# Performance work log

Measured on AMD Instinct MI355X. Metric: run time of the kernel, lower is better.

The kernel has to match this reference:

```python
import jax, jax.numpy as jnp
import numpy as np

BS = 4096
D = 256
TAU = 0.5
EPS = 1e-08          # eps added to negative-sum denominator (module arg)
COS_EPS = 1e-08      # nn.CosineSimilarity norm clamp


def setup_inputs() -> dict:
    key = jax.random.key(0)
    k1, k2 = jax.random.split(key)
    zi = jax.random.normal(k1, (BS, D), dtype=jnp.float32)
    zj = jax.random.normal(k2, (BS, D), dtype=jnp.float32)
    return {"zi": zi, "zj": zj}


def reference(zi, zj):
    bs = zi.shape[0]
    n = 2 * bs
    z = jnp.concatenate([zi, zj], axis=0)                       # [2bs, D]
    # cosine similarity = normalized dot products (norms clamped like torch)
    norm = jnp.linalg.norm(z, axis=-1, keepdims=True)
    zn = z / jnp.maximum(norm, COS_EPS)
    sim = jnp.matmul(zn, zn.T) / TAU                            # [2bs, 2bs]
    e = jnp.exp(sim)
    # positive pairs: row i pairs with column (i+bs) mod 2bs
    rows = jnp.arange(n)
    pair = jnp.concatenate([jnp.arange(bs) + bs, jnp.arange(bs)])
    sim_pos = e[rows, pair]                                     # [2bs]
    # negatives: all entries in a row except the diagonal
    sim_neg_sum = e.sum(axis=-1) - jnp.diagonal(e)              # [2bs]
    loss = jnp.mean(-jnp.log(sim_pos / (sim_neg_sum + EPS)))
    return loss
```

## Files before the change

kernel.cpp:

```cpp
#include <hip/hip_runtime.h>
#include <hip/hip_bf16.h>


#define N_ROWS 8192
#define BSZ    4096
#define DIM    256
#define INV_TAU 2.0f
#define EPS_REF 1e-8f
#define COS_EPS 1e-8f
#define NG2     64
#define NBLK2   (NG2 * (NG2 + 1) / 2)

typedef __attribute__((ext_vector_type(4))) float f32x4;
typedef long long i64;
typedef union { int4 v; i64 d[2]; } pack16;

__global__ __launch_bounds__(256) void knorm(const float* __restrict__ zi,
                                             const float* __restrict__ zj,
                                             unsigned char* __restrict__ znsw,
                                             float* __restrict__ out) {
    __shared__ float lds[4096];
    __shared__ float nrm[16];
    const int rg = blockIdx.x;
    const int t  = threadIdx.x;
    const int row0 = rg * 16;
    if (rg == 0 && t == 0) out[0] = 0.f;

    #pragma unroll
    for (int s = 0; s < 4; ++s) {
        const int e = s * 1024 + t * 4;
        const int r = row0 + (e >> 8);
        const int k = e & 255;
        const float* src = (r < BSZ) ? zi + (size_t)r * DIM + k
                                     : zj + (size_t)(r - BSZ) * DIM + k;
        *(float4*)&lds[e] = *(const float4*)src;
    }
    __syncthreads();

    {
        const int r = t >> 4, p = t & 15;
        float ss = 0.f;
        #pragma unroll
        for (int j = 0; j < 16; ++j) { const float x = lds[r * 256 + p * 16 + j]; ss += x * x; }
        ss += __shfl_xor(ss, 1); ss += __shfl_xor(ss, 2);
        ss += __shfl_xor(ss, 4); ss += __shfl_xor(ss, 8);
        if (p == 0) nrm[r] = 1.0f / fmaxf(sqrtf(ss), COS_EPS);
    }
    __syncthreads();

    const int kbp = t >> 6, fl = t & 63;
    const int r16 = fl & 15, q = fl >> 4;
    const float inv = nrm[r16];
    int w[4];
    #pragma unroll
    for (int h = 0; h < 2; ++h) {
        const int kk = (2 * kbp + h) * 32 + q * 8;
        float f[8];
        #pragma unroll
        for (int j = 0; j < 8; ++j) f[j] = lds[r16 * 256 + kk + j] * inv;
        int a = 0, b = 0;
        a = __builtin_amdgcn_cvt_pk_fp8_f32(f[0], f[1], a, false);
        a = __builtin_amdgcn_cvt_pk_fp8_f32(f[2], f[3], a, true);
        b = __builtin_amdgcn_cvt_pk_fp8_f32(f[4], f[5], b, false);
        b = __builtin_amdgcn_cvt_pk_fp8_f32(f[6], f[7], b, true);
        w[h * 2] = a; w[h * 2 + 1] = b;
    }
    *(int4*)(znsw + ((size_t)(rg * 4 + kbp) * 64 + fl) * 16) = make_int4(w[0], w[1], w[2], w[3]);
}

__global__ __launch_bounds__(256, 2) void kgemm(const unsigned char* __restrict__ znsw,
                                                float* __restrict__ P,
                                                float* __restrict__ selfdot,
                                                float* __restrict__ pairdot) {
    __shared__ __align__(16) unsigned char pan[2][32768];
    const int w = threadIdx.x >> 6;
    const int l = threadIdx.x & 63;

    const int t = blockIdx.x;
    int Gi = (int)((129.0f - sqrtf(16641.0f - 8.0f * (float)t)) * 0.5f);
    while ((Gi + 1) * (129 - (Gi + 1)) / 2 <= t) ++Gi;
    while (Gi * (129 - Gi) / 2 > t) --Gi;
    const int Gj = Gi + (t - Gi * (129 - Gi) / 2);

    const char* srcA = (const char*)znsw + (size_t)Gi * 32768;
    const char* srcB = (const char*)znsw + (size_t)Gj * 32768;
    #pragma unroll
    for (int sub = 0; sub < 8; ++sub) {
        const int off = sub * 4096 + w * 1024;
        __builtin_amdgcn_global_load_lds(
            (const __attribute__((address_space(1))) void*)(srcA + off + l * 16),
            (__attribute__((address_space(3))) void*)(&pan[0][off]), 16, 0, 0);
        __builtin_amdgcn_global_load_lds(
            (const __attribute__((address_space(1))) void*)(srcB + off + l * 16),
            (__attribute__((address_space(3))) void*)(&pan[1][off]), 16, 0, 0);
    }
    __syncthreads();

    const int rh = w >> 1, ch = w & 1;
    const char* Ap = (const char*)&pan[0][0] + rh * 16384 + l * 16;
    const char* Bp = (const char*)&pan[1][0] + ch * 16384 + l * 16;

    f32x4 acc[4][4];
    #pragma unroll
    for (int mt = 0; mt < 4; ++mt)
        #pragma unroll
        for (int nt = 0; nt < 4; ++nt)
            acc[mt][nt] = (f32x4){0.f, 0.f, 0.f, 0.f};

    #pragma unroll
    for (int kbp = 0; kbp < 4; ++kbp) {
        pack16 a4[4], b4[4];
        #pragma unroll
        for (int mt = 0; mt < 4; ++mt) a4[mt].v = *(const int4*)(Ap + (mt * 4 + kbp) * 1024);
        #pragma unroll
        for (int nt = 0; nt < 4; ++nt) b4[nt].v = *(const int4*)(Bp + (nt * 4 + kbp) * 1024);
        #pragma unroll
        for (int mt = 0; mt < 4; ++mt)
            #pragma unroll
            for (int nt = 0; nt < 4; ++nt) {
                acc[mt][nt] = __builtin_amdgcn_mfma_f32_16x16x32_fp8_fp8(
                    a4[mt].d[0], b4[nt].d[0], acc[mt][nt], 0, 0, 0);
                acc[mt][nt] = __builtin_amdgcn_mfma_f32_16x16x32_fp8_fp8(
                    a4[mt].d[1], b4[nt].d[1], acc[mt][nt], 0, 0, 0);
            }
    }

    const int c = l & 15, q = l >> 4;
    const int rsel = c - 4 * q;
    const bool vld = (rsel >= 0) && (rsel < 4);

    if ((Gi == Gj || Gj == Gi + 32) && rh == ch) {
        float dv[4];
        #pragma unroll
        for (int mt = 0; mt < 4; ++mt) {
            float d = acc[mt][mt][0];
            #pragma unroll
            for (int r = 1; r < 4; ++r)
                if (rsel == r) d = acc[mt][mt][r];
            dv[mt] = d;
        }
        if (vld) {
            float* dst = (Gi == Gj) ? selfdot : pairdot;
            #pragma unroll
            for (int mt = 0; mt < 4; ++mt)
                dst[Gi * 128 + rh * 64 + mt * 16 + c] = dv[mt];
        }
    }

    #pragma unroll
    for (int mt = 0; mt < 4; ++mt)
        #pragma unroll
        for (int nt = 0; nt < 4; ++nt)
            #pragma unroll
            for (int r = 0; r < 4; ++r)
                acc[mt][nt][r] = __expf(acc[mt][nt][r] * INV_TAU);

    float rs[4][4];
    #pragma unroll
    for (int mt = 0; mt < 4; ++mt)
        #pragma unroll
        for (int r = 0; r < 4; ++r)
            rs[mt][r] = acc[mt][0][r] + acc[mt][1][r] + acc[mt][2][r] + acc[mt][3][r];
    #pragma unroll
    for (int off = 1; off <= 8; off <<= 1)
        #pragma unroll
        for (int mt = 0; mt < 4; ++mt)
            #pragma unroll
            for (int r = 0; r < 4; ++r)
                rs[mt][r] += __shfl_xor(rs[mt][r], off);
    if (c == 0) {
        #pragma unroll
        for (int mt = 0; mt < 4; ++mt) {
            const f32x4 o4 = (f32x4){rs[mt][0], rs[mt][1], rs[mt][2], rs[mt][3]};
            __builtin_nontemporal_store(o4,
                (f32x4*)&P[(size_t)(Gj * 2 + ch) * N_ROWS + Gi * 128 + rh * 64 + mt * 16 + q * 4]);
        }
    }

    if (Gi != Gj) {
        float cs[4];
        #pragma unroll
        for (int nt = 0; nt < 4; ++nt) {
            float s = 0.f;
            #pragma unroll
            for (int mt = 0; mt < 4; ++mt)
                #pragma unroll
                for (int r = 0; r < 4; ++r)
                    s += acc[mt][nt][r];
            s += __shfl_xor(s, 16);
            s += __shfl_xor(s, 32);
            cs[nt] = s;
        }
        if (q == 0) {
            #pragma unroll
            for (int nt = 0; nt < 4; ++nt)
                __builtin_nontemporal_store(cs[nt],
                    &P[(size_t)(Gi * 2 + rh) * N_ROWS + Gj * 128 + ch * 64 + nt * 16 + c]);
        }
    }
}

__global__ __launch_bounds__(256) void kfinal(const float* __restrict__ P,
                                              const float* __restrict__ selfdot,
                                              const float* __restrict__ pairdot,
                                              float* __restrict__ out) {
    const int l = threadIdx.x & 63;
    const int w = threadIdx.x >> 6;
    const int row = blockIdx.x * 64 + l;
    float s = 0.f;
    #pragma unroll
    for (int st = 0; st < 32; ++st)
        s += P[(size_t)(w * 32 + st) * N_ROWS + row];
    __shared__ float wsum[4][64];
    wsum[w][l] = s;
    __syncthreads();
    if (w == 0) {
        const float tot = wsum[0][l] + wsum[1][l] + wsum[2][l] + wsum[3][l];
        const float selfe = __expf(selfdot[row] * INV_TAU);
        const float pd    = pairdot[(row < BSZ) ? row : row - BSZ];
        float loss = logf(tot - selfe + EPS_REF) - pd * INV_TAU;
        #pragma unroll
        for (int off = 32; off >= 1; off >>= 1) loss += __shfl_xor(loss, off);
        if (l == 0) atomicAdd(out, loss * (1.0f / (float)N_ROWS));
    }
}

extern "C" void kernel_launch(void* const* d_in, const int* in_sizes, int n_in,
                              void* d_out, int out_size, void* d_ws, size_t ws_size,
                              hipStream_t stream) {
    const float* zi = (const float*)d_in[0];
    const float* zj = (const float*)d_in[1];
    float* out = (float*)d_out;

    char* ws = (char*)d_ws;
    unsigned char* znsw = (unsigned char*)ws;
    float* P       = (float*)(ws + 2 * 1024 * 1024);
    float* selfdot = (float*)(ws + 6 * 1024 * 1024);
    float* pairdot = (float*)(ws + 6 * 1024 * 1024 + 32 * 1024);

    knorm <<<N_ROWS / 16, 256, 0, stream>>>(zi, zj, znsw, out);
    kgemm <<<NBLK2, 256, 0, stream>>>(znsw, P, selfdot, pairdot);
    kfinal<<<N_ROWS / 64, 256, 0, stream>>>(P, selfdot, pairdot, out);
}
```

Before: 89.43 us.

## Fuse norm, GEMM and final reduction into one cooperative persistent kernel

Replaces the three separate launches (normalize/quantize, FP8 GEMM+exp row sums, final loss reduction) with a single cooperative kernel of 512 persistent blocks, separated by grid-wide syncs. The GEMM tiles are looped over with a triangular index computation. The intent is to remove the per-kernel launch overhead and tail gaps. The cost is two grid barriers, fewer blocks than tiles (so up to five tile iterations per block with a barrier between them), and plain instead of nontemporal stores. The original three-kernel path is kept as a fallback if the cooperative launch fails.

```diff
diff --git a/kernel.cpp b/kernel.cpp
--- a/kernel.cpp
+++ b/kernel.cpp
@@ -1,5 +1,8 @@
 #include <hip/hip_runtime.h>
 #include <hip/hip_bf16.h>
+#include <hip/hip_cooperative_groups.h>
+
+namespace cg = cooperative_groups;
 
 
 #define N_ROWS 8192
@@ -9,11 +12,226 @@
 #define EPS_REF 1e-8f
 #define COS_EPS 1e-8f
 #define NG2     64
-#define NBLK2   (NG2 * (NG2 + 1) / 2)
+#define NTILES  (NG2 * (NG2 + 1) / 2)
+#define GRID    512
 
 typedef __attribute__((ext_vector_type(4))) float f32x4;
 typedef long long i64;
 typedef union { int4 v; i64 d[2]; } pack16;
+
+__global__ __launch_bounds__(256, 2) void kfused(const float* __restrict__ zi,
+                                                 const float* __restrict__ zj,
+                                                 unsigned char* __restrict__ znsw,
+                                                 float* __restrict__ P,
+                                                 float* __restrict__ selfdot,
+                                                 float* __restrict__ pairdot,
+                                                 float* __restrict__ out) {
+    __shared__ union {
+        struct { float lds[4096]; float nrm[16]; } p1;
+        struct { unsigned char pan[2][32768]; } p3;
+        struct { float wsum[4][64]; } p5;
+    } sm;
+
+    const int bid = blockIdx.x;
+    const int tid = threadIdx.x;
+    const int w   = tid >> 6;
+    const int l   = tid & 63;
+    cg::grid_group grid = cg::this_grid();
+
+    {
+        const int rg = bid;
+        const int row0 = rg * 16;
+        if (rg == 0 && tid == 0) out[0] = 0.f;
+
+        #pragma unroll
+        for (int s = 0; s < 4; ++s) {
+            const int e = s * 1024 + tid * 4;
+            const int r = row0 + (e >> 8);
+            const int k = e & 255;
+            const float* src = (r < BSZ) ? zi + (size_t)r * DIM + k
+                                         : zj + (size_t)(r - BSZ) * DIM + k;
+            *(float4*)&sm.p1.lds[e] = *(const float4*)src;
+        }
+        __syncthreads();
+        {
+            const int r = tid >> 4, p = tid & 15;
+            float ss = 0.f;
+            #pragma unroll
+            for (int j = 0; j < 16; ++j) { const float x = sm.p1.lds[r * 256 + p * 16 + j]; ss += x * x; }
+            ss += __shfl_xor(ss, 1); ss += __shfl_xor(ss, 2);
+            ss += __shfl_xor(ss, 4); ss += __shfl_xor(ss, 8);
+            if (p == 0) sm.p1.nrm[r] = 1.0f / fmaxf(sqrtf(ss), COS_EPS);
+        }
+        __syncthreads();
+        const int kbp = tid >> 6, fl = tid & 63;
+        const int r16 = fl & 15, q = fl >> 4;
+        const float inv = sm.p1.nrm[r16];
+        int wd[4];
+        #pragma unroll
+        for (int h = 0; h < 2; ++h) {
+            const int kk = (2 * kbp + h) * 32 + q * 8;
+            float f[8];
+            #pragma unroll
+            for (int j = 0; j < 8; ++j) f[j] = sm.p1.lds[r16 * 256 + kk + j] * inv;
+            int a = 0, b = 0;
+            a = __builtin_amdgcn_cvt_pk_fp8_f32(f[0], f[1], a, false);
+            a = __builtin_amdgcn_cvt_pk_fp8_f32(f[2], f[3], a, true);
+            b = __builtin_amdgcn_cvt_pk_fp8_f32(f[4], f[5], b, false);
+            b = __builtin_amdgcn_cvt_pk_fp8_f32(f[6], f[7], b, true);
+            wd[h * 2] = a; wd[h * 2 + 1] = b;
+        }
+        __syncthreads();
+        *(int4*)(znsw + ((size_t)(rg * 4 + kbp) * 64 + fl) * 16) =
+            make_int4(wd[0], wd[1], wd[2], wd[3]);
+    }
+
+    grid.sync();
+
+    for (int t = bid; t < NTILES; t += GRID) {
+        int Gi = (int)((129.0f - sqrtf(16641.0f - 8.0f * (float)t)) * 0.5f);
+        while ((Gi + 1) * (129 - (Gi + 1)) / 2 <= t) ++Gi;
+        while (Gi * (129 - Gi) / 2 > t) --Gi;
+        const int Gj = Gi + (t - Gi * (129 - Gi) / 2);
+
+        const char* srcA = (const char*)znsw + (size_t)Gi * 32768;
+        const char* srcB = (const char*)znsw + (size_t)Gj * 32768;
+        #pragma unroll
+        for (int sub = 0; sub < 8; ++sub) {
+            const int off = sub * 4096 + w * 1024;
+            __builtin_amdgcn_global_load_lds(
+                (const __attribute__((address_space(1))) void*)(srcA + off + l * 16),
+                (__attribute__((address_space(3))) void*)(&sm.p3.pan[0][off]), 16, 0, 0);
+            __builtin_amdgcn_global_load_lds(
+                (const __attribute__((address_space(1))) void*)(srcB + off + l * 16),
+                (__attribute__((address_space(3))) void*)(&sm.p3.pan[1][off]), 16, 0, 0);
+        }
+        __syncthreads();
+
+        const int rh = w >> 1, ch = w & 1;
+        const char* Ap = (const char*)&sm.p3.pan[0][0] + rh * 16384 + l * 16;
+        const char* Bp = (const char*)&sm.p3.pan[1][0] + ch * 16384 + l * 16;
+
+        f32x4 acc[4][4];
+        #pragma unroll
+        for (int mt = 0; mt < 4; ++mt)
+            #pragma unroll
+            for (int nt = 0; nt < 4; ++nt)
+                acc[mt][nt] = (f32x4){0.f, 0.f, 0.f, 0.f};
+
+        #pragma unroll
+        for (int kbp = 0; kbp < 4; ++kbp) {
+            pack16 a4[4], b4[4];
+            #pragma unroll
+            for (int mt = 0; mt < 4; ++mt) a4[mt].v = *(const int4*)(Ap + (mt * 4 + kbp) * 1024);
+            #pragma unroll
+            for (int nt = 0; nt < 4; ++nt) b4[nt].v = *(const int4*)(Bp + (nt * 4 + kbp) * 1024);
+            #pragma unroll
+            for (int mt = 0; mt < 4; ++mt)
+                #pragma unroll
+                for (int nt = 0; nt < 4; ++nt) {
+                    acc[mt][nt] = __builtin_amdgcn_mfma_f32_16x16x32_fp8_fp8(
+                        a4[mt].d[0], b4[nt].d[0], acc[mt][nt], 0, 0, 0);
+                    acc[mt][nt] = __builtin_amdgcn_mfma_f32_16x16x32_fp8_fp8(
+                        a4[mt].d[1], b4[nt].d[1], acc[mt][nt], 0, 0, 0);
+                }
+        }
+
+        const int c = l & 15, q = l >> 4;
+        const int rsel = c - 4 * q;
+        const bool vld = (rsel >= 0) && (rsel < 4);
+
+        if ((Gi == Gj || Gj == Gi + 32) && rh == ch) {
+            float dv[4];
+            #pragma unroll
+            for (int mt = 0; mt < 4; ++mt) {
+                float d = acc[mt][mt][0];
+                #pragma unroll
+                for (int r = 1; r < 4; ++r)
+                    if (rsel == r) d = acc[mt][mt][r];
+                dv[mt] = d;
+            }
+            if (vld) {
+                float* dst = (Gi == Gj) ? selfdot : pairdot;
+                #pragma unroll
+                for (int mt = 0; mt < 4; ++mt)
+                    dst[Gi * 128 + rh * 64 + mt * 16 + c] = dv[mt];
+            }
+        }
+
+        #pragma unroll
+        for (int mt = 0; mt < 4; ++mt)
+            #pragma unroll
+            for (int nt = 0; nt < 4; ++nt)
+                #pragma unroll
+                for (int r = 0; r < 4; ++r)
+                    acc[mt][nt][r] = __expf(acc[mt][nt][r] * INV_TAU);
+
+        float rs[4][4];
+        #pragma unroll
+        for (int mt = 0; mt < 4; ++mt)
+            #pragma unroll
+            for (int r = 0; r < 4; ++r)
+                rs[mt][r] = acc[mt][0][r] + acc[mt][1][r] + acc[mt][2][r] + acc[mt][3][r];
+        #pragma unroll
+        for (int off = 1; off <= 8; off <<= 1)
+            #pragma unroll
+            for (int mt = 0; mt < 4; ++mt)
+                #pragma unroll
+                for (int r = 0; r < 4; ++r)
+                    rs[mt][r] += __shfl_xor(rs[mt][r], off);
+        if (c == 0) {
+            #pragma unroll
+            for (int mt = 0; mt < 4; ++mt) {
+                const f32x4 o4 = (f32x4){rs[mt][0], rs[mt][1], rs[mt][2], rs[mt][3]};
+                *(f32x4*)&P[(size_t)(Gj * 2 + ch) * N_ROWS + Gi * 128 + rh * 64 + mt * 16 + q * 4] = o4;
+            }
+        }
+
+        if (Gi != Gj) {
+            float cs[4];
+            #pragma unroll
+            for (int nt = 0; nt < 4; ++nt) {
+                float s = 0.f;
+                #pragma unroll
+                for (int mt = 0; mt < 4; ++mt)
+                    #pragma unroll
+                    for (int r = 0; r < 4; ++r)
+                        s += acc[mt][nt][r];
+                s += __shfl_xor(s, 16);
+                s += __shfl_xor(s, 32);
+                cs[nt] = s;
+            }
+            if (q == 0) {
+                #pragma unroll
+                for (int nt = 0; nt < 4; ++nt)
+                    P[(size_t)(Gi * 2 + rh) * N_ROWS + Gj * 128 + ch * 64 + nt * 16 + c] = cs[nt];
+            }
+        }
+        __syncthreads();
+    }
+
+    grid.sync();
+
+    if (bid < N_ROWS / 64) {
+        const int row = bid * 64 + l;
+        float s = 0.f;
+        #pragma unroll
+        for (int st = 0; st < 32; ++st)
+            s += P[(size_t)(w * 32 + st) * N_ROWS + row];
+        sm.p5.wsum[w][l] = s;
+        __syncthreads();
+        if (w == 0) {
+            const float tot = sm.p5.wsum[0][l] + sm.p5.wsum[1][l]
+                            + sm.p5.wsum[2][l] + sm.p5.wsum[3][l];
+            const float selfe = __expf(selfdot[row] * INV_TAU);
+            const float pd    = pairdot[(row < BSZ) ? row : row - BSZ];
+            float loss = logf(tot - selfe + EPS_REF) - pd * INV_TAU;
+            #pragma unroll
+            for (int off = 32; off >= 1; off >>= 1) loss += __shfl_xor(loss, off);
+            if (l == 0) atomicAdd(out, loss * (1.0f / (float)N_ROWS));
+        }
+    }
+}
 
 __global__ __launch_bounds__(256) void knorm(const float* __restrict__ zi,
                                              const float* __restrict__ zj,
@@ -36,7 +254,6 @@
         *(float4*)&lds[e] = *(const float4*)src;
     }
     __syncthreads();
-
     {
         const int r = t >> 4, p = t & 15;
         float ss = 0.f;
@@ -47,7 +264,6 @@
         if (p == 0) nrm[r] = 1.0f / fmaxf(sqrtf(ss), COS_EPS);
     }
     __syncthreads();
-
     const int kbp = t >> 6, fl = t & 63;
     const int r16 = fl & 15, q = fl >> 4;
     const float inv = nrm[r16];
@@ -172,8 +388,7 @@
         #pragma unroll
         for (int mt = 0; mt < 4; ++mt) {
             const f32x4 o4 = (f32x4){rs[mt][0], rs[mt][1], rs[mt][2], rs[mt][3]};
-            __builtin_nontemporal_store(o4,
-                (f32x4*)&P[(size_t)(Gj * 2 + ch) * N_ROWS + Gi * 128 + rh * 64 + mt * 16 + q * 4]);
+            *(f32x4*)&P[(size_t)(Gj * 2 + ch) * N_ROWS + Gi * 128 + rh * 64 + mt * 16 + q * 4] = o4;
         }
     }
 
@@ -194,8 +409,7 @@
         if (q == 0) {
             #pragma unroll
             for (int nt = 0; nt < 4; ++nt)
-                __builtin_nontemporal_store(cs[nt],
-                    &P[(size_t)(Gi * 2 + rh) * N_ROWS + Gj * 128 + ch * 64 + nt * 16 + c]);
+                P[(size_t)(Gi * 2 + rh) * N_ROWS + Gj * 128 + ch * 64 + nt * 16 + c] = cs[nt];
         }
     }
 }
@@ -238,7 +452,13 @@
     float* selfdot = (float*)(ws + 6 * 1024 * 1024);
     float* pairdot = (float*)(ws + 6 * 1024 * 1024 + 32 * 1024);
 
-    knorm <<<N_ROWS / 16, 256, 0, stream>>>(zi, zj, znsw, out);
-    kgemm <<<NBLK2, 256, 0, stream>>>(znsw, P, selfdot, pairdot);
-    kfinal<<<N_ROWS / 64, 256, 0, stream>>>(P, selfdot, pairdot, out);
+    void* args[] = {(void*)&zi, (void*)&zj, (void*)&znsw, (void*)&P,
+                    (void*)&selfdot, (void*)&pairdot, (void*)&out};
+    hipError_t err = hipLaunchCooperativeKernel((void*)kfused, dim3(GRID),
+                                                dim3(256), args, 0, stream);
+    if (err != hipSuccess) {
+        knorm <<<N_ROWS / 16, 256, 0, stream>>>(zi, zj, znsw, out);
+        kgemm <<<NTILES, 256, 0, stream>>>(znsw, P, selfdot, pairdot);
+        kfinal<<<N_ROWS / 64, 256, 0, stream>>>(P, selfdot, pairdot, out);
+    }
 }
```

Result: slower. 190.4 us (+112.9%).

## Load B panel directly to registers with prefetch, pad norm LDS, fuse norm reduction

Applied to the files above, without the earlier changes.

In the GEMM kernel only the A panel is staged in LDS. The B fragments are read straight from global memory into registers, and the next k-slice is prefetched one step ahead. This halves LDS use so launch bounds can allow three blocks per CU. The norm kernel computes row sums of squares with a wave reduction during the load, which removes a barrier, and pads LDS rows to avoid bank conflicts. The risk is more global-memory latency and register pressure in the GEMM loop.

```diff
diff --git a/kernel.cpp b/kernel.cpp
--- a/kernel.cpp
+++ b/kernel.cpp
@@ -9,7 +9,8 @@
 #define EPS_REF 1e-8f
 #define COS_EPS 1e-8f
 #define NG2     64
-#define NBLK2   (NG2 * (NG2 + 1) / 2)
+#define NTILES  (NG2 * (NG2 + 1) / 2)
+#define LSTRIDE 260
 
 typedef __attribute__((ext_vector_type(4))) float f32x4;
 typedef long long i64;
@@ -19,60 +20,56 @@
                                              const float* __restrict__ zj,
                                              unsigned char* __restrict__ znsw,
                                              float* __restrict__ out) {
-    __shared__ float lds[4096];
+    __shared__ float lds[16 * LSTRIDE];
     __shared__ float nrm[16];
     const int rg = blockIdx.x;
     const int t  = threadIdx.x;
+    const int w  = t >> 6;
+    const int l  = t & 63;
     const int row0 = rg * 16;
     if (rg == 0 && t == 0) out[0] = 0.f;
 
     #pragma unroll
     for (int s = 0; s < 4; ++s) {
-        const int e = s * 1024 + t * 4;
-        const int r = row0 + (e >> 8);
-        const int k = e & 255;
-        const float* src = (r < BSZ) ? zi + (size_t)r * DIM + k
-                                     : zj + (size_t)(r - BSZ) * DIM + k;
-        *(float4*)&lds[e] = *(const float4*)src;
+        const int row = s * 4 + w;
+        const int r   = row0 + row;
+        const float* src = (r < BSZ) ? zi + (size_t)r * DIM + l * 4
+                                     : zj + (size_t)(r - BSZ) * DIM + l * 4;
+        const float4 v = *(const float4*)src;
+        *(float4*)&lds[row * LSTRIDE + l * 4] = v;
+        float ss = v.x*v.x + v.y*v.y + v.z*v.z + v.w*v.w;
+        #pragma unroll
+        for (int off = 32; off >= 1; off >>= 1) ss += __shfl_xor(ss, off);
+        if (l == 0) nrm[row] = 1.0f / fmaxf(sqrtf(ss), COS_EPS);
     }
     __syncthreads();
 
-    {
-        const int r = t >> 4, p = t & 15;
-        float ss = 0.f;
-        #pragma unroll
-        for (int j = 0; j < 16; ++j) { const float x = lds[r * 256 + p * 16 + j]; ss += x * x; }
-        ss += __shfl_xor(ss, 1); ss += __shfl_xor(ss, 2);
-        ss += __shfl_xor(ss, 4); ss += __shfl_xor(ss, 8);
-        if (p == 0) nrm[r] = 1.0f / fmaxf(sqrtf(ss), COS_EPS);
-    }
-    __syncthreads();
-
-    const int kbp = t >> 6, fl = t & 63;
+    const int kbp = w, fl = l;
     const int r16 = fl & 15, q = fl >> 4;
     const float inv = nrm[r16];
-    int w[4];
+    int wd[4];
     #pragma unroll
     for (int h = 0; h < 2; ++h) {
         const int kk = (2 * kbp + h) * 32 + q * 8;
         float f[8];
         #pragma unroll
-        for (int j = 0; j < 8; ++j) f[j] = lds[r16 * 256 + kk + j] * inv;
+        for (int j = 0; j < 8; ++j) f[j] = lds[r16 * LSTRIDE + kk + j] * inv;
         int a = 0, b = 0;
         a = __builtin_amdgcn_cvt_pk_fp8_f32(f[0], f[1], a, false);
         a = __builtin_amdgcn_cvt_pk_fp8_f32(f[2], f[3], a, true);
         b = __builtin_amdgcn_cvt_pk_fp8_f32(f[4], f[5], b, false);
         b = __builtin_amdgcn_cvt_pk_fp8_f32(f[6], f[7], b, true);
-        w[h * 2] = a; w[h * 2 + 1] = b;
-    }
-    *(int4*)(znsw + ((size_t)(rg * 4 + kbp) * 64 + fl) * 16) = make_int4(w[0], w[1], w[2], w[3]);
-}
-
-__global__ __launch_bounds__(256, 2) void kgemm(const unsigned char* __restrict__ znsw,
+        wd[h * 2] = a; wd[h * 2 + 1] = b;
+    }
+    *(int4*)(znsw + ((size_t)(rg * 4 + kbp) * 64 + fl) * 16) =
+        make_int4(wd[0], wd[1], wd[2], wd[3]);
+}
+
+__global__ __launch_bounds__(256, 3) void kgemm(const unsigned char* __restrict__ znsw,
                                                 float* __restrict__ P,
                                                 float* __restrict__ selfdot,
                                                 float* __restrict__ pairdot) {
-    __shared__ __align__(16) unsigned char pan[2][32768];
+    __shared__ __align__(16) unsigned char pan[32768];
     const int w = threadIdx.x >> 6;
     const int l = threadIdx.x & 63;
 
@@ -83,22 +80,22 @@
     const int Gj = Gi + (t - Gi * (129 - Gi) / 2);
 
     const char* srcA = (const char*)znsw + (size_t)Gi * 32768;
-    const char* srcB = (const char*)znsw + (size_t)Gj * 32768;
     #pragma unroll
     for (int sub = 0; sub < 8; ++sub) {
         const int off = sub * 4096 + w * 1024;
         __builtin_amdgcn_global_load_lds(
             (const __attribute__((address_space(1))) void*)(srcA + off + l * 16),
-            (__attribute__((address_space(3))) void*)(&pan[0][off]), 16, 0, 0);
-        __builtin_amdgcn_global_load_lds(
-            (const __attribute__((address_space(1))) void*)(srcB + off + l * 16),
-            (__attribute__((address_space(3))) void*)(&pan[1][off]), 16, 0, 0);
-    }
-    __syncthreads();
+            (__attribute__((address_space(3))) void*)(&pan[off]), 16, 0, 0);
+    }
 
     const int rh = w >> 1, ch = w & 1;
-    const char* Ap = (const char*)&pan[0][0] + rh * 16384 + l * 16;
-    const char* Bp = (const char*)&pan[1][0] + ch * 16384 + l * 16;
+    const char* Ap    = (const char*)&pan[0] + rh * 16384 + l * 16;
+    const char* bbase = (const char*)znsw + (size_t)Gj * 32768 + ch * 16384 + l * 16;
+
+    pack16 Bcur[4], Bnxt[4];
+    #pragma unroll
+    for (int nt = 0; nt < 4; ++nt)
+        Bcur[nt].v = *(const int4*)(bbase + nt * 4096);
 
     f32x4 acc[4][4];
     #pragma unroll
@@ -107,22 +104,30 @@
         for (int nt = 0; nt < 4; ++nt)
             acc[mt][nt] = (f32x4){0.f, 0.f, 0.f, 0.f};
 
+    __syncthreads();
+
     #pragma unroll
     for (int kbp = 0; kbp < 4; ++kbp) {
-        pack16 a4[4], b4[4];
-        #pragma unroll
-        for (int mt = 0; mt < 4; ++mt) a4[mt].v = *(const int4*)(Ap + (mt * 4 + kbp) * 1024);
-        #pragma unroll
-        for (int nt = 0; nt < 4; ++nt) b4[nt].v = *(const int4*)(Bp + (nt * 4 + kbp) * 1024);
+        if (kbp < 3) {
+            #pragma unroll
+            for (int nt = 0; nt < 4; ++nt)
+                Bnxt[nt].v = *(const int4*)(bbase + nt * 4096 + (kbp + 1) * 1024);
+        }
+        pack16 Afr[4];
+        #pragma unroll
+        for (int mt = 0; mt < 4; ++mt)
+            Afr[mt].v = *(const int4*)(Ap + mt * 4096 + kbp * 1024);
         #pragma unroll
         for (int mt = 0; mt < 4; ++mt)
             #pragma unroll
             for (int nt = 0; nt < 4; ++nt) {
                 acc[mt][nt] = __builtin_amdgcn_mfma_f32_16x16x32_fp8_fp8(
-                    a4[mt].d[0], b4[nt].d[0], acc[mt][nt], 0, 0, 0);
+                    Afr[mt].d[0], Bcur[nt].d[0], acc[mt][nt], 0, 0, 0);
                 acc[mt][nt] = __builtin_amdgcn_mfma_f32_16x16x32_fp8_fp8(
-                    a4[mt].d[1], b4[nt].d[1], acc[mt][nt], 0, 0, 0);
+                    Afr[mt].d[1], Bcur[nt].d[1], acc[mt][nt], 0, 0, 0);
             }
+        #pragma unroll
+        for (int nt = 0; nt < 4; ++nt) Bcur[nt] = Bnxt[nt];
     }
 
     const int c = l & 15, q = l >> 4;
@@ -239,6 +244,6 @@
     float* pairdot = (float*)(ws + 6 * 1024 * 1024 + 32 * 1024);
 
     knorm <<<N_ROWS / 16, 256, 0, stream>>>(zi, zj, znsw, out);
-    kgemm <<<NBLK2, 256, 0, stream>>>(znsw, P, selfdot, pairdot);
+    kgemm <<<NTILES, 256, 0, stream>>>(znsw, P, selfdot, pairdot);
     kfinal<<<N_ROWS / 64, 256, 0, stream>>>(P, selfdot, pairdot, out);
 }
```

Result: faster. 86.43 us (-3.4%).
